# Kernel tuning notes

Hardware: AMD Instinct MI355X
Metric: run time of the kernel (lower is better)

Reference implementation:

```python
import jax, jax.numpy as jnp
import numpy as np

B, N, H, A = 2048, 49, 1024, 512


def setup_inputs() -> dict:
    key = jax.random.key(0)
    ks = jax.random.split(key, 9)
    s_h = 1.0 / np.sqrt(H)
    s_a = 1.0 / np.sqrt(A)
    return {
        "hidden": jax.random.normal(ks[0], (B, H), jnp.float32),
        "img_features": jax.random.normal(ks[1], (B, N, H), jnp.float32),
        "coverage": jax.random.uniform(ks[2], (B, N), jnp.float32),
        "W_h": jax.random.uniform(ks[3], (H, A), jnp.float32, -s_h, s_h),
        "b_h": jax.random.uniform(ks[4], (A,), jnp.float32, -s_h, s_h),
        "W_img": jax.random.uniform(ks[5], (H, A), jnp.float32, -s_h, s_h),
        "b_img": jax.random.uniform(ks[6], (A,), jnp.float32, -s_h, s_h),
        "W_cov": jax.random.uniform(ks[7], (1, A), jnp.float32, -1.0, 1.0),
        "v": jax.random.uniform(ks[8], (A,), jnp.float32, -s_a, s_a),
    }


def reference(hidden, img_features, coverage, W_h, b_h, W_img, b_img, W_cov, v):
    # h_proj: (B, 1, A); img_proj: (B, N, A)
    h_proj = (hidden @ W_h + b_h)[:, None, :]
    img_proj = jnp.einsum("bnh,ha->bna", img_features, W_img) + b_img
    # coverage projection: (B, N, 1) @ (1, A) -> (B, N, A)
    cov_proj = coverage[:, :, None] * W_cov[0]
    energy = jnp.tanh(h_proj + img_proj + cov_proj)
    scores = jnp.einsum("bna,a->bn", energy, v)  # (B, N)
    alpha = jax.nn.softmax(scores, axis=1)
    context = jnp.einsum("bn,bnh->bh", alpha, img_features)
    return (context, alpha)
```

## Files before the change

kernel.cpp:

```cpp
#include <hip/hip_runtime.h>
#include <cstdint>
#include <cstddef>

#define B_ 2048
#define N_ 49
#define H_ 1024
#define A_ 512
#define M_ (B_*N_)

typedef __attribute__((ext_vector_type(8))) short short8;
typedef __attribute__((ext_vector_type(8))) unsigned short ushort8;
typedef __attribute__((ext_vector_type(4))) float f32x4;
typedef unsigned int u32;

__device__ inline unsigned short f2bf(float f){
  union { float f; unsigned u; } v; v.f = f;
  unsigned r = v.u + 0x7FFFu + ((v.u >> 16) & 1u);
  return (unsigned short)(r >> 16);
}
__device__ inline float bf2f(unsigned short h){
  union { u32 u; float f; } v; v.u = ((u32)h) << 16; return v.f;
}
__device__ inline float fast_tanh(float x){
  float e = __expf(2.0f*x);
  return 1.0f - 2.0f/(e + 1.0f);
}
__device__ inline void gl16(const void* g, void* l){
  __builtin_amdgcn_global_load_lds((const __attribute__((address_space(1))) u32*)g,
                                   (__attribute__((address_space(3))) u32*)l, 16, 0, 0);
}

__global__ __launch_bounds__(256) void k_transpose(
    const float* __restrict__ Wh, const float* __restrict__ Wimg,
    unsigned short* __restrict__ WtH, unsigned short* __restrict__ WtImg){
  const float* src = blockIdx.y ? Wimg : Wh;
  unsigned short* dst = blockIdx.y ? WtImg : WtH;
  int tk = (blockIdx.x & 31) * 32;
  int ta = (blockIdx.x >> 5) * 32;
  __shared__ unsigned short tile[32][33];
  int t = threadIdx.x;
  int r = t >> 3, c4 = t & 7;
  float4 vv = *(const float4*)(src + (size_t)(tk + r)*A_ + ta + c4*4);
  tile[c4*4+0][r] = f2bf(vv.x);
  tile[c4*4+1][r] = f2bf(vv.y);
  tile[c4*4+2][r] = f2bf(vv.z);
  tile[c4*4+3][r] = f2bf(vv.w);
  __syncthreads();
  ushort4 o;
  o.x = tile[r][c4*4+0]; o.y = tile[r][c4*4+1];
  o.z = tile[r][c4*4+2]; o.w = tile[r][c4*4+3];
  *(ushort4*)(dst + (size_t)(ta + r)*H_ + tk + c4*4) = o;
}

__global__ __launch_bounds__(256) void k_convert(
    const float* __restrict__ src, unsigned short* __restrict__ dst, size_t n8){
  size_t i = (size_t)blockIdx.x*256 + threadIdx.x;
  size_t stride = (size_t)gridDim.x*256;
  const float4* s4 = (const float4*)src;
  ushort8* d8 = (ushort8*)dst;
  for (; i < n8; i += stride){
    float4 a = s4[2*i], b = s4[2*i+1];
    ushort8 o;
    o[0]=f2bf(a.x); o[1]=f2bf(a.y); o[2]=f2bf(a.z); o[3]=f2bf(a.w);
    o[4]=f2bf(b.x); o[5]=f2bf(b.y); o[6]=f2bf(b.z); o[7]=f2bf(b.w);
    d8[i] = o;
  }
}

#define BK 64
#define LDK 72

__device__ inline void gemm_tile(const float* __restrict__ Asrc,
                                 const unsigned short* __restrict__ Wt,
                                 int m0, int a0, f32x4 acc[4][4],
                                 unsigned short (*sA)[LDK], unsigned short (*sB)[LDK]){
  const int t = threadIdx.x;
  const int l = t & 63, w = t >> 6;
  const int wr = w >> 1, wc = w & 1;
  const int g = l >> 4, c = l & 15;
  #pragma unroll
  for (int m=0;m<4;m++)
    #pragma unroll
    for (int n=0;n<4;n++)
      acc[m][n] = f32x4{0.f,0.f,0.f,0.f};

  for (int k0 = 0; k0 < H_; k0 += BK){
    #pragma unroll
    for (int i=0;i<8;i++){
      int f = i*256 + t;
      int row = f >> 4, c4 = f & 15;
      float4 vv = *(const float4*)(Asrc + (size_t)(m0+row)*H_ + k0 + c4*4);
      ushort4 h; h.x=f2bf(vv.x); h.y=f2bf(vv.y); h.z=f2bf(vv.z); h.w=f2bf(vv.w);
      *(ushort4*)&sA[row][c4*4] = h;
    }
    #pragma unroll
    for (int i=0;i<8;i++){
      int f = i*256 + t;
      int row = f >> 4, c4 = f & 15;
      *(ushort4*)&sB[row][c4*4] = *(const ushort4*)(Wt + (size_t)(a0+row)*H_ + k0 + c4*4);
    }
    __syncthreads();
    #pragma unroll
    for (int kk=0; kk<BK; kk+=32){
      short8 aF[4], bF[4];
      #pragma unroll
      for (int m=0;m<4;m++) aF[m] = *(const short8*)&sA[wr*64 + m*16 + c][kk + g*8];
      #pragma unroll
      for (int n=0;n<4;n++) bF[n] = *(const short8*)&sB[wc*64 + n*16 + c][kk + g*8];
      #pragma unroll
      for (int m=0;m<4;m++)
        #pragma unroll
        for (int n=0;n<4;n++)
          acc[m][n] = __builtin_amdgcn_mfma_f32_16x16x32_bf16(aF[m], bF[n], acc[m][n], 0, 0, 0);
    }
    __syncthreads();
  }
}

__global__ __launch_bounds__(256) void k_hproj(
    const float* __restrict__ hidden, const unsigned short* __restrict__ WtH,
    const float* __restrict__ b_h, float* __restrict__ hproj){
  __shared__ __align__(16) unsigned short sA[128][LDK];
  __shared__ __align__(16) unsigned short sB[128][LDK];
  f32x4 acc[4][4];
  int m0 = blockIdx.x * 128, a0 = blockIdx.y * 128;
  gemm_tile(hidden, WtH, m0, a0, acc, sA, sB);
  const int l = threadIdx.x & 63, w = threadIdx.x >> 6;
  const int wr = w >> 1, wc = w & 1, g = l >> 4, c = l & 15;
  #pragma unroll
  for (int n=0;n<4;n++){
    int col = a0 + wc*64 + n*16 + c;
    float bh = b_h[col];
    #pragma unroll
    for (int m=0;m<4;m++)
      #pragma unroll
      for (int r=0;r<4;r++){
        int rowg = m0 + wr*64 + m*16 + g*4 + r;
        hproj[(size_t)rowg*A_ + col] = acc[m][n][r] + bh;
      }
  }
}

__global__ __launch_bounds__(512, 2) void k_scores_b8(
    const unsigned short* __restrict__ Ab, const unsigned short* __restrict__ Wt,
    const float* __restrict__ hproj, const float* __restrict__ b_img,
    const float* __restrict__ cov, const float* __restrict__ Wcov,
    const float* __restrict__ v, float* __restrict__ scoresP){
  __shared__ __align__(16) char lds[131072];
  const int t = threadIdx.x;
  const int l = t & 63, w = t >> 6;
  const int wr = w >> 2, wc = w & 3;
  const int g = l >> 4, c = l & 15;
  const int cm = (c & 7) << 4;

  const int nwg = (M_/256)*(A_/256);
  int bid = blockIdx.x;
  int wg = (bid & 7)*(nwg/8) + (bid >> 3);
  const int m0 = (wg >> 1) * 256;
  const int a0 = (wg & 1) * 256;

  const int rsub = l >> 3;
  const int ksw  = ((l & 7) ^ rsub) * 8;

  f32x4 acc[8][4] = {};

  auto stage = [&](int bn, int k0){
    #pragma unroll
    for (int h=0; h<2; h++){
      #pragma unroll
      for (int q=0; q<2; q++){
        int dA = bn*65536 + h*16384 + w*2048 + q*1024;
        const unsigned short* ga = Ab + (size_t)(m0 + h*128 + w*16 + q*8 + rsub)*H_ + k0 + ksw;
        const unsigned short* gb = Wt + (size_t)(a0 + h*128 + w*16 + q*8 + rsub)*H_ + k0 + ksw;
        gl16(ga, lds + dA);
        gl16(gb, lds + dA + 32768);
      }
    }
  };

  const int abase = wr*16384;
  const int bbase = 32768 + (wc>>1)*16384;
  const int brow  = (wc&1)*64;

  stage(0, 0);
  for (int tt=0; tt<16; tt++){
    const int cur = (tt & 1) << 16;
    if (tt < 15){
      stage((tt+1)&1, (tt+1)*64);
      asm volatile("s_waitcnt vmcnt(8)" ::: "memory");
    } else {
      asm volatile("s_waitcnt vmcnt(0)" ::: "memory");
    }
    asm volatile("s_barrier" ::: "memory");
    #pragma unroll
    for (int p=0; p<4; p++){
      const int mh  = p >> 1;
      const int kb  = (p & 1) * 64;
      short8 aF[4], bF[4];
      #pragma unroll
      for (int i=0;i<4;i++){
        int rl = (mh*4+i)*16 + c;
        aF[i] = *(const short8*)(lds + cur + abase + rl*128 + ((kb + g*16) ^ cm));
      }
      #pragma unroll
      for (int n=0;n<4;n++){
        int rb = brow + n*16 + c;
        bF[n] = *(const short8*)(lds + cur + bbase + rb*128 + ((kb + g*16) ^ cm));
      }
      asm volatile("s_barrier" ::: "memory");
      __builtin_amdgcn_s_setprio(1);
      #pragma unroll
      for (int i=0;i<4;i++)
        #pragma unroll
        for (int n=0;n<4;n++)
          acc[mh*4+i][n] = __builtin_amdgcn_mfma_f32_16x16x32_bf16(aF[i], bF[n], acc[mh*4+i][n], 0, 0, 0);
      __builtin_amdgcn_s_setprio(0);
      asm volatile("s_barrier" ::: "memory");
    }
  }

  float* sS = (float*)lds;
  float* sH = (float*)lds + 256;
  const int bFirst = m0 / N_;
  const int nB = (m0 + 255)/N_ - bFirst + 1;
  if (t < 256) sS[t] = 0.f;
  for (int idx = t; idx < nB*256; idx += 512){
    int bb = idx >> 8, a = idx & 255;
    sH[bb*256 + a] = hproj[(size_t)(bFirst + bb)*A_ + a0 + a];
  }
  __syncthreads();

  float vv[4], bi[4], wcv[4];
  #pragma unroll
  for (int n=0;n<4;n++){
    int colg = a0 + wc*64 + n*16 + c;
    vv[n] = v[colg]; bi[n] = b_img[colg]; wcv[n] = Wcov[colg];
  }
  #pragma unroll
  for (int m=0;m<8;m++){
    #pragma unroll
    for (int r=0;r<4;r++){
      int rowl = wr*128 + m*16 + g*4 + r;
      int rowg = m0 + rowl;
      int bb = rowg / N_ - bFirst;
      float cv = cov[rowg];
      float s = 0.f;
      #pragma unroll
      for (int n=0;n<4;n++){
        float x = acc[m][n][r] + sH[bb*256 + wc*64 + n*16 + c] + bi[n] + cv*wcv[n];
        s += fast_tanh(x) * vv[n];
      }
      s += __shfl_xor(s, 1, 16);
      s += __shfl_xor(s, 2, 16);
      s += __shfl_xor(s, 4, 16);
      s += __shfl_xor(s, 8, 16);
      if (c == 0) atomicAdd(&sS[rowl], s);
    }
  }
  __syncthreads();
  if (t < 256) scoresP[(size_t)(a0 >> 8)*M_ + m0 + t] = sS[t];
}

__global__ __launch_bounds__(256) void k_scores_f(
    const float* __restrict__ img, const unsigned short* __restrict__ WtImg,
    const float* __restrict__ hproj, const float* __restrict__ b_img,
    const float* __restrict__ cov, const float* __restrict__ Wcov,
    const float* __restrict__ v, float* __restrict__ scores){
  __shared__ __align__(16) unsigned short sA[128][LDK];
  __shared__ __align__(16) unsigned short sB[128][LDK];
  __shared__ float sH[4][128];
  f32x4 acc[4][4];
  int m0 = blockIdx.x * 128, a0 = blockIdx.y * 128;
  gemm_tile(img, WtImg, m0, a0, acc, sA, sB);
  int bFirst = m0 / N_;
  int bLast  = (m0 + 127) / N_;
  int nB = bLast - bFirst + 1;
  for (int idx = threadIdx.x; idx < nB*128; idx += 256){
    int bb = idx >> 7, a = idx & 127;
    sH[bb][a] = hproj[(size_t)(bFirst + bb)*A_ + a0 + a];
  }
  __syncthreads();
  const int l = threadIdx.x & 63, w = threadIdx.x >> 6;
  const int wr = w >> 1, wc = w & 1, g = l >> 4, c = l & 15;
  float vv[4], bi[4], wcv[4];
  #pragma unroll
  for (int n=0;n<4;n++){
    int col = a0 + wc*64 + n*16 + c;
    vv[n] = v[col]; bi[n] = b_img[col]; wcv[n] = Wcov[col];
  }
  #pragma unroll
  for (int m=0;m<4;m++)
    #pragma unroll
    for (int r=0;r<4;r++){
      int rowg = m0 + wr*64 + m*16 + g*4 + r;
      int bb = rowg / N_;
      float cv = cov[rowg];
      float s = 0.f;
      #pragma unroll
      for (int n=0;n<4;n++){
        float x = acc[m][n][r] + sH[bb - bFirst][wc*64 + n*16 + c] + bi[n] + cv*wcv[n];
        s += fast_tanh(x) * vv[n];
      }
      s += __shfl_xor(s, 1, 16);
      s += __shfl_xor(s, 2, 16);
      s += __shfl_xor(s, 4, 16);
      s += __shfl_xor(s, 8, 16);
      if (c == 0) atomicAdd(&scores[rowg], s);
    }
}

__global__ __launch_bounds__(256) void k_ctx_b(
    const unsigned short* __restrict__ imgb, const float* __restrict__ scoresP,
    float* __restrict__ outCtx, float* __restrict__ outAlpha){
  int b = blockIdx.x;
  __shared__ float sAl[N_];
  int t = threadIdx.x;
  if (t < 64){
    float s = -1e30f;
    if (t < N_){
      size_t rg = (size_t)b*N_ + t;
      s = scoresP[rg] + scoresP[(size_t)M_ + rg];
    }
    float m = s;
    #pragma unroll
    for (int off=32; off>=1; off>>=1) m = fmaxf(m, __shfl_xor(m, off));
    float e = (t < N_) ? __expf(s - m) : 0.f;
    float sum = e;
    #pragma unroll
    for (int off=32; off>=1; off>>=1) sum += __shfl_xor(sum, off);
    float al = e / sum;
    if (t < N_){ sAl[t] = al; outAlpha[(size_t)b*N_ + t] = al; }
  }
  __syncthreads();
  float4 acc = {0.f,0.f,0.f,0.f};
  #pragma unroll 7
  for (int n=0;n<N_;n++){
    float al = sAl[n];
    ushort4 x = *(const ushort4*)(imgb + ((size_t)b*N_ + n)*H_ + t*4);
    acc.x += al*bf2f(x.x); acc.y += al*bf2f(x.y);
    acc.z += al*bf2f(x.z); acc.w += al*bf2f(x.w);
  }
  *(float4*)(outCtx + (size_t)b*H_ + t*4) = acc;
}

__global__ __launch_bounds__(256) void k_ctx_f(
    const float* __restrict__ img, const float* __restrict__ scores,
    float* __restrict__ outCtx, float* __restrict__ outAlpha){
  int b = blockIdx.x;
  __shared__ float sAl[N_];
  int t = threadIdx.x;
  if (t < 64){
    float s = (t < N_) ? scores[(size_t)b*N_ + t] : -1e30f;
    float m = s;
    #pragma unroll
    for (int off=32; off>=1; off>>=1) m = fmaxf(m, __shfl_xor(m, off));
    float e = (t < N_) ? __expf(s - m) : 0.f;
    float sum = e;
    #pragma unroll
    for (int off=32; off>=1; off>>=1) sum += __shfl_xor(sum, off);
    float al = e / sum;
    if (t < N_){ sAl[t] = al; outAlpha[(size_t)b*N_ + t] = al; }
  }
  __syncthreads();
  const float4* ib = (const float4*)(img + (size_t)b*N_*H_);
  float4 acc = {0.f,0.f,0.f,0.f};
  for (int n=0;n<N_;n++){
    float al = sAl[n];
    float4 x = ib[n*(H_/4) + t];
    acc.x += al*x.x; acc.y += al*x.y; acc.z += al*x.z; acc.w += al*x.w;
  }
  *(float4*)(outCtx + (size_t)b*H_ + t*4) = acc;
}

extern "C" void kernel_launch(void* const* d_in, const int* in_sizes, int n_in,
                              void* d_out, int out_size, void* d_ws, size_t ws_size,
                              hipStream_t stream){
  const float* hidden = (const float*)d_in[0];
  const float* img    = (const float*)d_in[1];
  const float* cov    = (const float*)d_in[2];
  const float* W_h    = (const float*)d_in[3];
  const float* b_h    = (const float*)d_in[4];
  const float* W_img  = (const float*)d_in[5];
  const float* b_img  = (const float*)d_in[6];
  const float* W_cov  = (const float*)d_in[7];
  const float* v      = (const float*)d_in[8];

  char* ws = (char*)d_ws;
  unsigned short* WtH   = (unsigned short*)ws;
  unsigned short* WtImg = (unsigned short*)(ws + (1u<<20));
  float* hproj   = (float*)(ws + (2u<<20));
  float* scoresP = (float*)(ws + (6u<<20));
  unsigned short* imgb = (unsigned short*)(ws + (8u<<20));

  float* outCtx   = (float*)d_out;
  float* outAlpha = outCtx + (size_t)B_*H_;

  const size_t needed = (8ull<<20) + (size_t)M_*H_*2;

  k_transpose<<<dim3(512, 2), 256, 0, stream>>>(W_h, W_img, WtH, WtImg);
  k_hproj<<<dim3(B_/128, A_/128), 256, 0, stream>>>(hidden, WtH, b_h, hproj);

  if (ws_size >= needed){
    k_convert<<<2048, 256, 0, stream>>>(img, imgb, (size_t)M_*H_/8);
    k_scores_b8<<<(M_/256)*(A_/256), 512, 0, stream>>>(imgb, WtImg, hproj, b_img, cov, W_cov, v, scoresP);
    k_ctx_b<<<B_, 256, 0, stream>>>(imgb, scoresP, outCtx, outAlpha);
  } else {
    hipMemsetAsync(scoresP, 0, (size_t)M_*sizeof(float), stream);
    k_scores_f<<<dim3(M_/128, A_/128), 256, 0, stream>>>(img, WtImg, hproj, b_img, cov, W_cov, v, scoresP);
    k_ctx_f<<<B_, 256, 0, stream>>>(img, scoresP, outCtx, outAlpha);
  }
}
```

Before: 381.9 us.

## Fuse bf16 conversion, score GEMM, softmax and context into one kernel

Replaces the separate convert, score-GEMM and context kernels with a single kernel. Each block owns 5 whole batches (245 rows): it converts fp32 image features to bf16 while staging them into LDS and writing them back to global memory, then runs both 256-wide halves of the A dimension in turn. Scores stay in shared memory, so softmax and the context reduction happen in the same block. This removes the standalone conversion pass, the global scores round trip and two launches. In exchange, 11 of every 256 tile rows are padding, the grid shrinks to 410 large blocks (a possible load-imbalance tail), and the ctx loop does narrower ushort2 loads.

```diff
diff --git a/kernel.cpp b/kernel.cpp
--- a/kernel.cpp
+++ b/kernel.cpp
@@ -7,6 +7,8 @@
 #define H_ 1024
 #define A_ 512
 #define M_ (B_*N_)
+#define NBB 5
+#define NBLK ((B_ + NBB - 1)/NBB)
 
 typedef __attribute__((ext_vector_type(8))) short short8;
 typedef __attribute__((ext_vector_type(8))) unsigned short ushort8;
@@ -52,21 +54,6 @@
   *(ushort4*)(dst + (size_t)(ta + r)*H_ + tk + c4*4) = o;
 }
 
-__global__ __launch_bounds__(256) void k_convert(
-    const float* __restrict__ src, unsigned short* __restrict__ dst, size_t n8){
-  size_t i = (size_t)blockIdx.x*256 + threadIdx.x;
-  size_t stride = (size_t)gridDim.x*256;
-  const float4* s4 = (const float4*)src;
-  ushort8* d8 = (ushort8*)dst;
-  for (; i < n8; i += stride){
-    float4 a = s4[2*i], b = s4[2*i+1];
-    ushort8 o;
-    o[0]=f2bf(a.x); o[1]=f2bf(a.y); o[2]=f2bf(a.z); o[3]=f2bf(a.w);
-    o[4]=f2bf(b.x); o[5]=f2bf(b.y); o[6]=f2bf(b.z); o[7]=f2bf(b.w);
-    d8[i] = o;
-  }
-}
-
 #define BK 64
 #define LDK 72
 
@@ -141,124 +128,232 @@
   }
 }
 
-__global__ __launch_bounds__(512, 2) void k_scores_b8(
-    const unsigned short* __restrict__ Ab, const unsigned short* __restrict__ Wt,
-    const float* __restrict__ hproj, const float* __restrict__ b_img,
-    const float* __restrict__ cov, const float* __restrict__ Wcov,
-    const float* __restrict__ v, float* __restrict__ scoresP){
+__global__ __launch_bounds__(512, 2) void k_fused(
+    const float* __restrict__ img, unsigned short* __restrict__ imgb,
+    const unsigned short* __restrict__ Wt, const float* __restrict__ hproj,
+    const float* __restrict__ b_img, const float* __restrict__ cov,
+    const float* __restrict__ Wcov, const float* __restrict__ v,
+    float* __restrict__ outCtx, float* __restrict__ outAlpha){
   __shared__ __align__(16) char lds[131072];
+  __shared__ float sS[256];
+  __shared__ float sH[NBB][256];
+  __shared__ float sAl[256];
+
   const int t = threadIdx.x;
   const int l = t & 63, w = t >> 6;
   const int wr = w >> 2, wc = w & 3;
   const int g = l >> 4, c = l & 15;
   const int cm = (c & 7) << 4;
 
-  const int nwg = (M_/256)*(A_/256);
-  int bid = blockIdx.x;
-  int wg = (bid & 7)*(nwg/8) + (bid >> 3);
-  const int m0 = (wg >> 1) * 256;
-  const int a0 = (wg & 1) * 256;
+  const int bm = blockIdx.x;
+  const int bb0 = bm * NBB;
+  const int NB = min(NBB, B_ - bb0);
+  const int mrows = NB * N_;
+  const int m0 = bb0 * N_;
+
+  if (t < 256) sS[t] = 0.f;
 
   const int rsub = l >> 3;
   const int ksw  = ((l & 7) ^ rsub) * 8;
-
-  f32x4 acc[8][4] = {};
-
-  auto stage = [&](int bn, int k0){
-    #pragma unroll
-    for (int h=0; h<2; h++){
-      #pragma unroll
-      for (int q=0; q<2; q++){
-        int dA = bn*65536 + h*16384 + w*2048 + q*1024;
-        const unsigned short* ga = Ab + (size_t)(m0 + h*128 + w*16 + q*8 + rsub)*H_ + k0 + ksw;
-        const unsigned short* gb = Wt + (size_t)(a0 + h*128 + w*16 + q*8 + rsub)*H_ + k0 + ksw;
-        gl16(ga, lds + dA);
-        gl16(gb, lds + dA + 32768);
-      }
-    }
+  const int arow = t >> 1, akq = t & 1;
+  const int arC  = (arow < mrows) ? arow : 0;
+
+  f32x4 acc[8][4];
+
+  auto stageB = [&](int bn, int k0, int a0){
+    #pragma unroll
+    for (int h=0;h<2;h++)
+      #pragma unroll
+      for (int q=0;q<2;q++){
+        int row = h*128 + w*16 + q*8 + rsub;
+        gl16(Wt + (size_t)(a0 + row)*H_ + k0 + ksw,
+             lds + bn*65536 + 32768 + h*16384 + w*2048 + q*1024);
+      }
   };
-
-  const int abase = wr*16384;
-  const int bbase = 32768 + (wc>>1)*16384;
-  const int brow  = (wc&1)*64;
-
-  stage(0, 0);
-  for (int tt=0; tt<16; tt++){
+  auto stageA2 = [&](int bn, int k0){
+    #pragma unroll
+    for (int h=0;h<2;h++)
+      #pragma unroll
+      for (int q=0;q<2;q++){
+        int row = h*128 + w*16 + q*8 + rsub;
+        int rr = (row < mrows) ? row : 0;
+        gl16(imgb + (size_t)(m0 + rr)*H_ + k0 + ksw,
+             lds + bn*65536 + h*16384 + w*2048 + q*1024);
+      }
+  };
+
+  auto compute = [&](int tt){
     const int cur = (tt & 1) << 16;
-    if (tt < 15){
-      stage((tt+1)&1, (tt+1)*64);
-      asm volatile("s_waitcnt vmcnt(8)" ::: "memory");
-    } else {
-      asm volatile("s_waitcnt vmcnt(0)" ::: "memory");
-    }
+    const int abase = cur + wr*16384;
+    const int bbase = cur + 32768 + (wc>>1)*16384;
+    const int brow  = (wc & 1)*64;
+    #pragma unroll
+    for (int kb2=0; kb2<2; ++kb2){
+      const int ko = kb2*64;
+      short8 bF[4];
+      #pragma unroll
+      for (int n=0;n<4;n++)
+        bF[n] = *(const short8*)(lds + bbase + (brow + n*16 + c)*128 + ((ko + g*16) ^ cm));
+      #pragma unroll
+      for (int mh=0; mh<2; ++mh){
+        short8 aF[4];
+        #pragma unroll
+        for (int i=0;i<4;i++)
+          aF[i] = *(const short8*)(lds + abase + ((mh*4+i)*16 + c)*128 + ((ko + g*16) ^ cm));
+        __builtin_amdgcn_s_setprio(1);
+        #pragma unroll
+        for (int i=0;i<4;i++)
+          #pragma unroll
+          for (int n=0;n<4;n++)
+            acc[mh*4+i][n] = __builtin_amdgcn_mfma_f32_16x16x32_bf16(aF[i], bF[n], acc[mh*4+i][n], 0, 0, 0);
+        __builtin_amdgcn_s_setprio(0);
+      }
+    }
+  };
+
+  auto epilogue = [&](int a0){
+    for (int idx = t; idx < NB*256; idx += 512){
+      int bb = idx >> 8, a = idx & 255;
+      sH[bb][a] = hproj[(size_t)(bb0 + bb)*A_ + a0 + a];
+    }
+    asm volatile("s_waitcnt lgkmcnt(0)" ::: "memory");
     asm volatile("s_barrier" ::: "memory");
-    #pragma unroll
-    for (int p=0; p<4; p++){
-      const int mh  = p >> 1;
-      const int kb  = (p & 1) * 64;
-      short8 aF[4], bF[4];
-      #pragma unroll
-      for (int i=0;i<4;i++){
-        int rl = (mh*4+i)*16 + c;
-        aF[i] = *(const short8*)(lds + cur + abase + rl*128 + ((kb + g*16) ^ cm));
-      }
-      #pragma unroll
-      for (int n=0;n<4;n++){
-        int rb = brow + n*16 + c;
-        bF[n] = *(const short8*)(lds + cur + bbase + rb*128 + ((kb + g*16) ^ cm));
-      }
+    float vv[4], bi[4], wcv[4];
+    #pragma unroll
+    for (int n=0;n<4;n++){
+      int colg = a0 + wc*64 + n*16 + c;
+      vv[n] = v[colg]; bi[n] = b_img[colg]; wcv[n] = Wcov[colg];
+    }
+    #pragma unroll
+    for (int m=0;m<8;m++){
+      #pragma unroll
+      for (int r=0;r<4;r++){
+        int rowl = wr*128 + m*16 + g*4 + r;
+        if (rowl < mrows){
+          int bb = rowl / N_;
+          float cv = cov[m0 + rowl];
+          float s = 0.f;
+          #pragma unroll
+          for (int n=0;n<4;n++){
+            float x = acc[m][n][r] + sH[bb][wc*64 + n*16 + c] + bi[n] + cv*wcv[n];
+            s += fast_tanh(x) * vv[n];
+          }
+          s += __shfl_xor(s, 1, 16);
+          s += __shfl_xor(s, 2, 16);
+          s += __shfl_xor(s, 4, 16);
+          s += __shfl_xor(s, 8, 16);
+          if (c == 0) atomicAdd(&sS[rowl], s);
+        }
+      }
+    }
+    asm volatile("s_waitcnt lgkmcnt(0)" ::: "memory");
+    asm volatile("s_barrier" ::: "memory");
+  };
+
+  {
+    #pragma unroll
+    for (int m=0;m<8;m++)
+      #pragma unroll
+      for (int n=0;n<4;n++)
+        acc[m][n] = f32x4{0.f,0.f,0.f,0.f};
+
+    float4 av[8];
+    auto loadA = [&](int k0){
+      const float4* asrc = (const float4*)(img + (size_t)(m0 + arC)*H_ + k0 + akq*32);
+      #pragma unroll
+      for (int i=0;i<8;i++) av[i] = asrc[i];
+    };
+    auto writeA = [&](int bn, int k0){
+      #pragma unroll
+      for (int j=0;j<4;j++){
+        ushort8 o;
+        o[0]=f2bf(av[2*j].x); o[1]=f2bf(av[2*j].y); o[2]=f2bf(av[2*j].z); o[3]=f2bf(av[2*j].w);
+        o[4]=f2bf(av[2*j+1].x); o[5]=f2bf(av[2*j+1].y); o[6]=f2bf(av[2*j+1].z); o[7]=f2bf(av[2*j+1].w);
+        int ch = akq*4 + j;
+        *(ushort8*)(lds + bn*65536 + arow*128 + ((ch*16) ^ ((arow&7)<<4))) = o;
+        if (arow < mrows)
+          *(ushort8*)(imgb + (size_t)(m0 + arow)*H_ + k0 + ch*8) = o;
+      }
+    };
+
+    loadA(0);
+    stageB(0, 0, 0);
+    asm volatile("s_waitcnt vmcnt(4)" ::: "memory");
+    writeA(0, 0);
+    for (int tt=0; tt<16; ++tt){
+      if (tt < 15){
+        loadA((tt+1)*64);
+        stageB((tt+1)&1, (tt+1)*64, 0);
+        asm volatile("s_waitcnt vmcnt(4)" ::: "memory");
+        writeA((tt+1)&1, (tt+1)*64);
+      } else {
+        asm volatile("s_waitcnt vmcnt(0)" ::: "memory");
+      }
+      asm volatile("s_waitcnt lgkmcnt(0)" ::: "memory");
       asm volatile("s_barrier" ::: "memory");
-      __builtin_amdgcn_s_setprio(1);
-      #pragma unroll
-      for (int i=0;i<4;i++)
-        #pragma unroll
-        for (int n=0;n<4;n++)
-          acc[mh*4+i][n] = __builtin_amdgcn_mfma_f32_16x16x32_bf16(aF[i], bF[n], acc[mh*4+i][n], 0, 0, 0);
-      __builtin_amdgcn_s_setprio(0);
+      compute(tt);
       asm volatile("s_barrier" ::: "memory");
     }
-  }
-
-  float* sS = (float*)lds;
-  float* sH = (float*)lds + 256;
-  const int bFirst = m0 / N_;
-  const int nB = (m0 + 255)/N_ - bFirst + 1;
-  if (t < 256) sS[t] = 0.f;
-  for (int idx = t; idx < nB*256; idx += 512){
-    int bb = idx >> 8, a = idx & 255;
-    sH[bb*256 + a] = hproj[(size_t)(bFirst + bb)*A_ + a0 + a];
-  }
-  __syncthreads();
-
-  float vv[4], bi[4], wcv[4];
-  #pragma unroll
-  for (int n=0;n<4;n++){
-    int colg = a0 + wc*64 + n*16 + c;
-    vv[n] = v[colg]; bi[n] = b_img[colg]; wcv[n] = Wcov[colg];
-  }
-  #pragma unroll
-  for (int m=0;m<8;m++){
-    #pragma unroll
-    for (int r=0;r<4;r++){
-      int rowl = wr*128 + m*16 + g*4 + r;
-      int rowg = m0 + rowl;
-      int bb = rowg / N_ - bFirst;
-      float cv = cov[rowg];
-      float s = 0.f;
-      #pragma unroll
-      for (int n=0;n<4;n++){
-        float x = acc[m][n][r] + sH[bb*256 + wc*64 + n*16 + c] + bi[n] + cv*wcv[n];
-        s += fast_tanh(x) * vv[n];
-      }
-      s += __shfl_xor(s, 1, 16);
-      s += __shfl_xor(s, 2, 16);
-      s += __shfl_xor(s, 4, 16);
-      s += __shfl_xor(s, 8, 16);
-      if (c == 0) atomicAdd(&sS[rowl], s);
-    }
-  }
-  __syncthreads();
-  if (t < 256) scoresP[(size_t)(a0 >> 8)*M_ + m0 + t] = sS[t];
+    epilogue(0);
+  }
+
+  {
+    #pragma unroll
+    for (int m=0;m<8;m++)
+      #pragma unroll
+      for (int n=0;n<4;n++)
+        acc[m][n] = f32x4{0.f,0.f,0.f,0.f};
+
+    stageA2(0, 0);
+    stageB(0, 0, 256);
+    for (int tt=0; tt<16; ++tt){
+      if (tt < 15){
+        stageA2((tt+1)&1, (tt+1)*64);
+        stageB((tt+1)&1, (tt+1)*64, 256);
+        asm volatile("s_waitcnt vmcnt(8)" ::: "memory");
+      } else {
+        asm volatile("s_waitcnt vmcnt(0)" ::: "memory");
+      }
+      asm volatile("s_barrier" ::: "memory");
+      compute(tt);
+      asm volatile("s_barrier" ::: "memory");
+    }
+    epilogue(256);
+  }
+
+  asm volatile("s_barrier" ::: "memory");
+  if (w < NB){
+    int b = w;
+    float s = (l < N_) ? sS[b*N_ + l] : -1e30f;
+    float mx = s;
+    #pragma unroll
+    for (int off=32; off>=1; off>>=1) mx = fmaxf(mx, __shfl_xor(mx, off));
+    float e = (l < N_) ? __expf(s - mx) : 0.f;
+    float sum = e;
+    #pragma unroll
+    for (int off=32; off>=1; off>>=1) sum += __shfl_xor(sum, off);
+    float al = e / sum;
+    if (l < N_){
+      sAl[b*N_ + l] = al;
+      outAlpha[(size_t)(m0 + b*N_ + l)] = al;
+    }
+  }
+  asm volatile("s_waitcnt lgkmcnt(0)" ::: "memory");
+  asm volatile("s_barrier" ::: "memory");
+
+  const ushort2* ib2 = (const ushort2*)imgb;
+  for (int b=0; b<NB; ++b){
+    float ax = 0.f, ay = 0.f;
+    #pragma unroll 7
+    for (int n=0; n<N_; ++n){
+      float al = sAl[b*N_ + n];
+      ushort2 u = ib2[(size_t)(m0 + b*N_ + n)*(H_/2) + t];
+      ax += al * bf2f(u.x);
+      ay += al * bf2f(u.y);
+    }
+    float2 o; o.x = ax; o.y = ay;
+    *(float2*)(outCtx + (size_t)(bb0 + b)*H_ + t*2) = o;
+  }
 }
 
 __global__ __launch_bounds__(256) void k_scores_f(
@@ -309,40 +404,6 @@
     }
 }
 
-__global__ __launch_bounds__(256) void k_ctx_b(
-    const unsigned short* __restrict__ imgb, const float* __restrict__ scoresP,
-    float* __restrict__ outCtx, float* __restrict__ outAlpha){
-  int b = blockIdx.x;
-  __shared__ float sAl[N_];
-  int t = threadIdx.x;
-  if (t < 64){
-    float s = -1e30f;
-    if (t < N_){
-      size_t rg = (size_t)b*N_ + t;
-      s = scoresP[rg] + scoresP[(size_t)M_ + rg];
-    }
-    float m = s;
-    #pragma unroll
-    for (int off=32; off>=1; off>>=1) m = fmaxf(m, __shfl_xor(m, off));
-    float e = (t < N_) ? __expf(s - m) : 0.f;
-    float sum = e;
-    #pragma unroll
-    for (int off=32; off>=1; off>>=1) sum += __shfl_xor(sum, off);
-    float al = e / sum;
-    if (t < N_){ sAl[t] = al; outAlpha[(size_t)b*N_ + t] = al; }
-  }
-  __syncthreads();
-  float4 acc = {0.f,0.f,0.f,0.f};
-  #pragma unroll 7
-  for (int n=0;n<N_;n++){
-    float al = sAl[n];
-    ushort4 x = *(const ushort4*)(imgb + ((size_t)b*N_ + n)*H_ + t*4);
-    acc.x += al*bf2f(x.x); acc.y += al*bf2f(x.y);
-    acc.z += al*bf2f(x.z); acc.w += al*bf2f(x.w);
-  }
-  *(float4*)(outCtx + (size_t)b*H_ + t*4) = acc;
-}
-
 __global__ __launch_bounds__(256) void k_ctx_f(
     const float* __restrict__ img, const float* __restrict__ scores,
     float* __restrict__ outCtx, float* __restrict__ outAlpha){
@@ -389,7 +450,7 @@
   unsigned short* WtH   = (unsigned short*)ws;
   unsigned short* WtImg = (unsigned short*)(ws + (1u<<20));
   float* hproj   = (float*)(ws + (2u<<20));
-  float* scoresP = (float*)(ws + (6u<<20));
+  float* scoresF = (float*)(ws + (6u<<20));
   unsigned short* imgb = (unsigned short*)(ws + (8u<<20));
 
   float* outCtx   = (float*)d_out;
@@ -401,12 +462,11 @@
   k_hproj<<<dim3(B_/128, A_/128), 256, 0, stream>>>(hidden, WtH, b_h, hproj);
 
   if (ws_size >= needed){
-    k_convert<<<2048, 256, 0, stream>>>(img, imgb, (size_t)M_*H_/8);
-    k_scores_b8<<<(M_/256)*(A_/256), 512, 0, stream>>>(imgb, WtImg, hproj, b_img, cov, W_cov, v, scoresP);
-    k_ctx_b<<<B_, 256, 0, stream>>>(imgb, scoresP, outCtx, outAlpha);
+    k_fused<<<NBLK, 512, 0, stream>>>(img, imgb, WtImg, hproj, b_img, cov, W_cov, v,
+                                      outCtx, outAlpha);
   } else {
-    hipMemsetAsync(scoresP, 0, (size_t)M_*sizeof(float), stream);
-    k_scores_f<<<dim3(M_/128, A_/128), 256, 0, stream>>>(img, WtImg, hproj, b_img, cov, W_cov, v, scoresP);
-    k_ctx_f<<<B_, 256, 0, stream>>>(img, scoresP, outCtx, outAlpha);
-  }
-}
+    hipMemsetAsync(scoresF, 0, (size_t)M_*sizeof(float), stream);
+    k_scores_f<<<dim3(M_/128, A_/128), 256, 0, stream>>>(img, WtImg, hproj, b_img, cov, W_cov, v, scoresF);
+    k_ctx_f<<<B_, 256, 0, stream>>>(img, scoresF, outCtx, outAlpha);
+  }
+}
```

Result: slower. 407.1 us (+6.6%).

## Interleave next-tile global loads with MFMA phases in scores GEMM

Applied to the files above, without the earlier changes.

Restructures the main GEMM loop of the bf16 scores kernel so the prefetch of the next K-tile is split into four chunks, each issued just before one of the four MFMA phases, with finer vmcnt waits. Each phase now waits on lgkmcnt and uses a sched_barrier before its MFMAs. The aim is to spread global-to-LDS traffic across the compute phases and reduce the burst stall at the start of each K step. It adds more barriers per iteration and depends on the vmcnt counts matching the new issue order. k_ctx_b is also moved to a different place in the file, which does not change its behaviour.

```diff
diff --git a/kernel.cpp b/kernel.cpp
--- a/kernel.cpp
+++ b/kernel.cpp
@@ -141,7 +141,7 @@
   }
 }
 
-__global__ __launch_bounds__(512, 2) void k_scores_b8(
+__global__ __launch_bounds__(512, 2) void k_scores_p8(
     const unsigned short* __restrict__ Ab, const unsigned short* __restrict__ Wt,
     const float* __restrict__ hproj, const float* __restrict__ b_img,
     const float* __restrict__ cov, const float* __restrict__ Wcov,
@@ -164,59 +164,73 @@
 
   f32x4 acc[8][4] = {};
 
-  auto stage = [&](int bn, int k0){
-    #pragma unroll
-    for (int h=0; h<2; h++){
-      #pragma unroll
-      for (int q=0; q<2; q++){
-        int dA = bn*65536 + h*16384 + w*2048 + q*1024;
-        const unsigned short* ga = Ab + (size_t)(m0 + h*128 + w*16 + q*8 + rsub)*H_ + k0 + ksw;
-        const unsigned short* gb = Wt + (size_t)(a0 + h*128 + w*16 + q*8 + rsub)*H_ + k0 + ksw;
-        gl16(ga, lds + dA);
-        gl16(gb, lds + dA + 32768);
-      }
-    }
+  auto unit = [&](int d, int opoff, int h, int row0,
+                  const unsigned short* src, int prow, int k0){
+    gl16(src + (size_t)(prow + h*128 + row0 + w*8 + rsub)*H_ + k0 + ksw,
+         lds + d*65536 + opoff + h*16384 + row0*128 + w*1024);
   };
 
-  const int abase = wr*16384;
-  const int bbase = 32768 + (wc>>1)*16384;
-  const int brow  = (wc&1)*64;
-
-  stage(0, 0);
-  for (int tt=0; tt<16; tt++){
+  const int abase_s = wr*16384;
+  const int bbase_s = 32768 + (wc>>1)*16384;
+  const int brow    = (wc & 1)*64;
+
+  auto phase_mfma = [&](int cur, int mh, int kb){
+    short8 aF[4], bF[4];
+    #pragma unroll
+    for (int i=0;i<4;i++)
+      aF[i] = *(const short8*)(lds + cur + abase_s + (mh*64 + i*16 + c)*128 + ((kb*64 + g*16) ^ cm));
+    #pragma unroll
+    for (int n=0;n<4;n++)
+      bF[n] = *(const short8*)(lds + cur + bbase_s + (brow + n*16 + c)*128 + ((kb*64 + g*16) ^ cm));
+    asm volatile("s_waitcnt lgkmcnt(0)" ::: "memory");
+    __builtin_amdgcn_sched_barrier(0);
+    __builtin_amdgcn_s_setprio(1);
+    #pragma unroll
+    for (int i=0;i<4;i++)
+      #pragma unroll
+      for (int n=0;n<4;n++)
+        acc[mh*4+i][n] = __builtin_amdgcn_mfma_f32_16x16x32_bf16(aF[i], bF[n], acc[mh*4+i][n], 0, 0, 0);
+    __builtin_amdgcn_s_setprio(0);
+  };
+
+  unit(0, 32768, 0, 0,  Wt, a0, 0);
+  unit(0, 32768, 0, 64, Wt, a0, 0);
+  unit(0, 32768, 1, 0,  Wt, a0, 0);
+  unit(0, 32768, 1, 64, Wt, a0, 0);
+  unit(0, 0,     0, 0,  Ab, m0, 0);
+  unit(0, 0,     1, 0,  Ab, m0, 0);
+  unit(0, 0,     0, 64, Ab, m0, 0);
+  unit(0, 0,     1, 64, Ab, m0, 0);
+
+  for (int tt=0; tt<16; ++tt){
     const int cur = (tt & 1) << 16;
-    if (tt < 15){
-      stage((tt+1)&1, (tt+1)*64);
-      asm volatile("s_waitcnt vmcnt(8)" ::: "memory");
-    } else {
-      asm volatile("s_waitcnt vmcnt(0)" ::: "memory");
-    }
-    asm volatile("s_barrier" ::: "memory");
-    #pragma unroll
-    for (int p=0; p<4; p++){
-      const int mh  = p >> 1;
-      const int kb  = (p & 1) * 64;
-      short8 aF[4], bF[4];
-      #pragma unroll
-      for (int i=0;i<4;i++){
-        int rl = (mh*4+i)*16 + c;
-        aF[i] = *(const short8*)(lds + cur + abase + rl*128 + ((kb + g*16) ^ cm));
-      }
-      #pragma unroll
-      for (int n=0;n<4;n++){
-        int rb = brow + n*16 + c;
-        bF[n] = *(const short8*)(lds + cur + bbase + rb*128 + ((kb + g*16) ^ cm));
-      }
-      asm volatile("s_barrier" ::: "memory");
-      __builtin_amdgcn_s_setprio(1);
-      #pragma unroll
-      for (int i=0;i<4;i++)
-        #pragma unroll
-        for (int n=0;n<4;n++)
-          acc[mh*4+i][n] = __builtin_amdgcn_mfma_f32_16x16x32_bf16(aF[i], bF[n], acc[mh*4+i][n], 0, 0, 0);
-      __builtin_amdgcn_s_setprio(0);
-      asm volatile("s_barrier" ::: "memory");
-    }
+    const int nd  = (tt + 1) & 1;
+    const int nk  = (tt + 1) * 64;
+    const bool pf = (tt < 15);
+
+    if (pf){ unit(nd, 32768, 0, 0, Wt, a0, nk); unit(nd, 32768, 0, 64, Wt, a0, nk);
+             asm volatile("s_waitcnt vmcnt(4)" ::: "memory"); }
+    else   { asm volatile("s_waitcnt vmcnt(2)" ::: "memory"); }
+    asm volatile("s_barrier" ::: "memory");
+    phase_mfma(cur, 0, 0);
+    asm volatile("s_barrier" ::: "memory");
+
+    if (pf){ unit(nd, 32768, 1, 0, Wt, a0, nk); unit(nd, 32768, 1, 64, Wt, a0, nk); }
+    asm volatile("s_barrier" ::: "memory");
+    phase_mfma(cur, 0, 1);
+    asm volatile("s_barrier" ::: "memory");
+
+    if (pf){ unit(nd, 0, 0, 0, Ab, m0, nk); unit(nd, 0, 1, 0, Ab, m0, nk);
+             asm volatile("s_waitcnt vmcnt(6)" ::: "memory"); }
+    else   { asm volatile("s_waitcnt vmcnt(0)" ::: "memory"); }
+    asm volatile("s_barrier" ::: "memory");
+    phase_mfma(cur, 1, 0);
+    asm volatile("s_barrier" ::: "memory");
+
+    if (pf){ unit(nd, 0, 0, 64, Ab, m0, nk); unit(nd, 0, 1, 64, Ab, m0, nk); }
+    asm volatile("s_barrier" ::: "memory");
+    phase_mfma(cur, 1, 1);
+    asm volatile("s_barrier" ::: "memory");
   }
 
   float* sS = (float*)lds;
@@ -241,9 +255,8 @@
     #pragma unroll
     for (int r=0;r<4;r++){
       int rowl = wr*128 + m*16 + g*4 + r;
-      int rowg = m0 + rowl;
-      int bb = rowg / N_ - bFirst;
-      float cv = cov[rowg];
+      int bb = (m0 + rowl) / N_ - bFirst;
+      float cv = cov[m0 + rowl];
       float s = 0.f;
       #pragma unroll
       for (int n=0;n<4;n++){
@@ -259,6 +272,40 @@
   }
   __syncthreads();
   if (t < 256) scoresP[(size_t)(a0 >> 8)*M_ + m0 + t] = sS[t];
+}
+
+__global__ __launch_bounds__(256) void k_ctx_b(
+    const unsigned short* __restrict__ imgb, const float* __restrict__ scoresP,
+    float* __restrict__ outCtx, float* __restrict__ outAlpha){
+  int b = blockIdx.x;
+  __shared__ float sAl[N_];
+  int t = threadIdx.x;
+  if (t < 64){
+    float s = -1e30f;
+    if (t < N_){
+      size_t rg = (size_t)b*N_ + t;
+      s = scoresP[rg] + scoresP[(size_t)M_ + rg];
+    }
+    float m = s;
+    #pragma unroll
+    for (int off=32; off>=1; off>>=1) m = fmaxf(m, __shfl_xor(m, off));
+    float e = (t < N_) ? __expf(s - m) : 0.f;
+    float sum = e;
+    #pragma unroll
+    for (int off=32; off>=1; off>>=1) sum += __shfl_xor(sum, off);
+    float al = e / sum;
+    if (t < N_){ sAl[t] = al; outAlpha[(size_t)b*N_ + t] = al; }
+  }
+  __syncthreads();
+  float4 acc = {0.f,0.f,0.f,0.f};
+  #pragma unroll 7
+  for (int n=0;n<N_;n++){
+    float al = sAl[n];
+    ushort4 x = *(const ushort4*)(imgb + ((size_t)b*N_ + n)*H_ + t*4);
+    acc.x += al*bf2f(x.x); acc.y += al*bf2f(x.y);
+    acc.z += al*bf2f(x.z); acc.w += al*bf2f(x.w);
+  }
+  *(float4*)(outCtx + (size_t)b*H_ + t*4) = acc;
 }
 
 __global__ __launch_bounds__(256) void k_scores_f(
@@ -309,40 +356,6 @@
     }
 }
 
-__global__ __launch_bounds__(256) void k_ctx_b(
-    const unsigned short* __restrict__ imgb, const float* __restrict__ scoresP,
-    float* __restrict__ outCtx, float* __restrict__ outAlpha){
-  int b = blockIdx.x;
-  __shared__ float sAl[N_];
-  int t = threadIdx.x;
-  if (t < 64){
-    float s = -1e30f;
-    if (t < N_){
-      size_t rg = (size_t)b*N_ + t;
-      s = scoresP[rg] + scoresP[(size_t)M_ + rg];
-    }
-    float m = s;
-    #pragma unroll
-    for (int off=32; off>=1; off>>=1) m = fmaxf(m, __shfl_xor(m, off));
-    float e = (t < N_) ? __expf(s - m) : 0.f;
-    float sum = e;
-    #pragma unroll
-    for (int off=32; off>=1; off>>=1) sum += __shfl_xor(sum, off);
-    float al = e / sum;
-    if (t < N_){ sAl[t] = al; outAlpha[(size_t)b*N_ + t] = al; }
-  }
-  __syncthreads();
-  float4 acc = {0.f,0.f,0.f,0.f};
-  #pragma unroll 7
-  for (int n=0;n<N_;n++){
-    float al = sAl[n];
-    ushort4 x = *(const ushort4*)(imgb + ((size_t)b*N_ + n)*H_ + t*4);
-    acc.x += al*bf2f(x.x); acc.y += al*bf2f(x.y);
-    acc.z += al*bf2f(x.z); acc.w += al*bf2f(x.w);
-  }
-  *(float4*)(outCtx + (size_t)b*H_ + t*4) = acc;
-}
-
 __global__ __launch_bounds__(256) void k_ctx_f(
     const float* __restrict__ img, const float* __restrict__ scores,
     float* __restrict__ outCtx, float* __restrict__ outAlpha){
@@ -402,7 +415,7 @@
 
   if (ws_size >= needed){
     k_convert<<<2048, 256, 0, stream>>>(img, imgb, (size_t)M_*H_/8);
-    k_scores_b8<<<(M_/256)*(A_/256), 512, 0, stream>>>(imgb, WtImg, hproj, b_img, cov, W_cov, v, scoresP);
+    k_scores_p8<<<(M_/256)*(A_/256), 512, 0, stream>>>(imgb, WtImg, hproj, b_img, cov, W_cov, v, scoresP);
     k_ctx_b<<<B_, 256, 0, stream>>>(imgb, scoresP, outCtx, outAlpha);
   } else {
     hipMemsetAsync(scoresP, 0, (size_t)M_*sizeof(float), stream);
```

Result: faster. 347.2 us, median of 4 (-9.1%).
